# Kernel optimization log

Hardware: AMD Instinct MI355X
Metric: run time of the kernel (lower is better)

## Reference

```python
import jax, jax.numpy as jnp
import numpy as np

D_MODEL = 1024
NUM_HEADS = 16
HEAD_DIM = D_MODEL // NUM_HEADS
MASK_FUTURE = False
NEG_INF = -1.0e9


def setup_inputs() -> dict:
    key = jax.random.key(0)
    ks = jax.random.split(key, 8)
    B, L = 2, 2048
    q = jax.random.normal(ks[0], (B, L, D_MODEL), dtype=jnp.float32)
    k = jax.random.normal(ks[1], (B, L, D_MODEL), dtype=jnp.float32)
    v = jax.random.normal(ks[2], (B, L, D_MODEL), dtype=jnp.float32)
    attention_mask = jnp.ones((B, L), dtype=jnp.int32)
    s = 1.0 / np.sqrt(D_MODEL)
    Wq = jax.random.normal(ks[3], (D_MODEL, D_MODEL), dtype=jnp.float32) * s
    Wk = jax.random.normal(ks[4], (D_MODEL, D_MODEL), dtype=jnp.float32) * s
    Wv = jax.random.normal(ks[5], (D_MODEL, D_MODEL), dtype=jnp.float32) * s
    Wo = jax.random.normal(ks[6], (D_MODEL, D_MODEL), dtype=jnp.float32) * s
    return {"q": q, "k": k, "v": v, "attention_mask": attention_mask,
            "Wq": Wq, "Wk": Wk, "Wv": Wv, "Wo": Wo}


def _split_heads(x):
    B, L, _ = x.shape
    return x.reshape(B, L, NUM_HEADS, HEAD_DIM).transpose(0, 2, 1, 3)  # [B,H,L,Hd]


def reference(q, k, v, attention_mask, Wq, Wk, Wv, Wo):
    B, Lq, _ = q.shape
    Lk = k.shape[1]
    Q = _split_heads(q @ Wq.T)
    K = _split_heads(k @ Wk.T)
    V = _split_heads(v @ Wv.T)
    scale = HEAD_DIM ** 0.5  # per-head D in original Attention
    scores = jnp.einsum('bhqd,bhkd->bhqk', Q, K) / scale
    mask = (attention_mask == 0)[:, None, None, :]  # [B,1,1,Lk]
    scores = jnp.where(mask, NEG_INF, scores)
    if MASK_FUTURE:
        fut = jnp.triu(jnp.ones((Lq, Lk), dtype=bool), k=1)
        scores = jnp.where(fut[None, None], NEG_INF, scores)
    attn = jax.nn.softmax(scores, axis=-1)
    out = jnp.einsum('bhqk,bhkd->bhqd', attn, V)
    out = out.transpose(0, 2, 1, 3).reshape(B, Lq, D_MODEL)
    return out @ Wo.T
```

## Files before the change

### kernel.cpp

```cpp
#include <hip/hip_runtime.h>


#define D_MODEL 1024
#define NH 16
#define HD 64
#define BATCH 2
#define SEQ 2048
#define MROWS (BATCH*SEQ)

typedef unsigned short u16;
typedef __bf16 bf16x8 __attribute__((ext_vector_type(8)));
typedef float f32x4 __attribute__((ext_vector_type(4)));
typedef float f32x16 __attribute__((ext_vector_type(16)));

__device__ __forceinline__ u16 f2bf(float f){
    __bf16 h = (__bf16)f;
    return __builtin_bit_cast(u16, h);
}
__device__ __forceinline__ float fast_exp2(float x){ return __builtin_amdgcn_exp2f(x); }

__device__ __forceinline__ void stage16(const void* g, void* l){
#if __has_builtin(__builtin_amdgcn_global_load_lds)
    __builtin_amdgcn_global_load_lds(
        (__attribute__((address_space(1))) void*)(unsigned long long)(g),
        (__attribute__((address_space(3))) void*)(unsigned int)(unsigned long long)(l),
        16, 0, 0);
#else
    *(uint4*)l = *(const uint4*)g;
#endif
}

__device__ __forceinline__ int detect_f32_block(const u16* q, int tid){
    __shared__ int flag;
    if (tid < 64){
        unsigned e = (q[2*tid]>>7)&0xFFu;
        bool hit = (e>=115u)&&(e<=132u);
        unsigned long long m = __ballot(hit);
        if (tid==0) flag = (__popcll(m) < 32) ? 1 : 0;
    }
    __syncthreads();
    return flag;
}

__global__ __launch_bounds__(256)
void convert_all(const u16* __restrict__ q, const u16* __restrict__ k,
                 const u16* __restrict__ v, const u16* __restrict__ Wq,
                 const u16* __restrict__ Wk, const u16* __restrict__ Wv,
                 const u16* __restrict__ Wo, u16* __restrict__ dst)
{
    int isf32 = detect_f32_block(q, threadIdx.x);
    int bid = blockIdx.x;
    const u16* src; int lb;
    if      (bid < 4096)  { src=q;  lb=bid; }
    else if (bid < 8192)  { src=k;  lb=bid-4096; }
    else if (bid < 12288) { src=v;  lb=bid-8192; }
    else if (bid < 13312) { src=Wq; lb=bid-12288; }
    else if (bid < 14336) { src=Wk; lb=bid-13312; }
    else if (bid < 15360) { src=Wv; lb=bid-14336; }
    else                  { src=Wo; lb=bid-15360; }
    size_t so = (size_t)lb*1024 + threadIdx.x*4;
    size_t dofs = (size_t)bid*1024 + threadIdx.x*4;
    if (isf32){
        float4 x = *(const float4*)((const float*)src + so);
        ushort4 o; o.x=f2bf(x.x); o.y=f2bf(x.y); o.z=f2bf(x.z); o.w=f2bf(x.w);
        *(ushort4*)(dst+dofs) = o;
    } else {
        *(ushort4*)(dst+dofs) = *(const ushort4*)(src+so);
    }
}

__global__ __launch_bounds__(512)
void gemm_qkv(const u16* __restrict__ qb, const u16* __restrict__ kb,
              const u16* __restrict__ vb, const u16* __restrict__ Wqb,
              const u16* __restrict__ Wkb, const u16* __restrict__ Wvb,
              u16* __restrict__ Qh, u16* __restrict__ Kh, u16* __restrict__ Vt)
{
    const int K = 1024;
    __shared__ __align__(16) u16 lA[2][128*64];
    __shared__ __align__(16) u16 lB[2][128*64];

    const int lid = blockIdx.x + 8*(blockIdx.y + 32*blockIdx.z);
    const int xcd = lid & 7, loc = lid >> 3;
    const int xb = loc & 7, p = loc >> 3;
    const int yz = xcd*12 + p;
    const int z = yz >> 5, yb = yz & 31;

    const u16* A  = (z==0)? qb  : (z==1)? kb  : vb;
    const u16* Bt = (z==0)? Wqb : (z==1)? Wkb : Wvb;

    const int tid  = threadIdx.x;
    const int wid  = tid>>6, lane = tid&63;
    const int quad = lane>>4, l16 = lane&15;
    const int wm = (wid&3)*32, wn = (wid>>2)*64;
    const int row0 = yb*128, col0 = xb*128;

    f32x4 acc[2][4];
    #pragma unroll
    for (int i=0;i<2;i++)
        #pragma unroll
        for (int j=0;j<4;j++) acc[i][j] = (f32x4){0.f,0.f,0.f,0.f};

    #define QKV_STAGE(buf, k0)                                                 \
        _Pragma("unroll")                                                      \
        for (int s=0;s<2;s++){                                                 \
            int c = tid + s*512;                                               \
            int row = c>>3, cr = c&7;                                          \
            int gc = cr ^ (row&7);                                             \
            stage16(&A [(size_t)(row0+row)*K + (k0) + gc*8], &lA[buf][c*8]);   \
            stage16(&Bt[(size_t)(col0+row)*K + (k0) + gc*8], &lB[buf][c*8]);   \
        }

    QKV_STAGE(0, 0)
    __syncthreads();

    int cur = 0;
    for (int t=0; t<16; ++t){
        if (t < 15) QKV_STAGE(cur^1, (t+1)*64)
        #pragma unroll
        for (int kk=0;kk<2;kk++){
            bf16x8 af[2], bfr[4];
            #pragma unroll
            for (int mi=0;mi<2;mi++){
                int r = wm + mi*16 + l16;
                af[mi] = *(const bf16x8*)&lA[cur][r*64 + ((kk*4+quad) ^ (r&7))*8];
            }
            #pragma unroll
            for (int ni=0;ni<4;ni++){
                int r = wn + ni*16 + l16;
                bfr[ni] = *(const bf16x8*)&lB[cur][r*64 + ((kk*4+quad) ^ (r&7))*8];
            }
            #pragma unroll
            for (int mi=0;mi<2;mi++)
                #pragma unroll
                for (int ni=0;ni<4;ni++)
                    acc[mi][ni] = __builtin_amdgcn_mfma_f32_16x16x32_bf16(af[mi], bfr[ni], acc[mi][ni], 0,0,0);
        }
        __syncthreads();
        cur ^= 1;
    }
    #undef QKV_STAGE

    const float qsc = (z==0) ? 0.18033688011112042f : 1.0f;
    u16* Csh = (z==0)? Qh : Kh;
    #pragma unroll
    for (int mi=0;mi<2;mi++){
        #pragma unroll
        for (int ni=0;ni<4;ni++){
            int col = col0 + wn + ni*16 + l16;
            #pragma unroll
            for (int r=0;r<4;r++){
                int row = row0 + wm + mi*16 + quad*4 + r;
                u16 o = f2bf(acc[mi][ni][r]*qsc);
                int b = row>>11, i = row&2047, h = col>>6, d = col&63;
                if (z<2) Csh[((((size_t)(b*NH+h))*SEQ + i)<<6) + d] = o;
                else     Vt[((size_t)((b*NH+h)*HD + d))*SEQ + i] = o;
            }
        }
    }
}

__global__ __launch_bounds__(512)
void gemm_out(const u16* __restrict__ A, const u16* __restrict__ Bt,
              void* __restrict__ Cv, const u16* __restrict__ qref)
{
    const int K = 1024, N = 1024;
    int outf32 = detect_f32_block(qref, threadIdx.x);
    __shared__ __align__(16) u16 lA[2][64*64];
    __shared__ __align__(16) u16 lB[2][128*64];
    const int tid  = threadIdx.x;
    const int wid  = tid>>6, lane = tid&63;
    const int quad = lane>>4, l16 = lane&15;
    const int wm = (wid&1)*32, wn = (wid>>1)*32;

    const int lid = blockIdx.x + 8*blockIdx.y;
    const int xcd = lid & 7, loc = lid >> 3;
    const int xb = loc & 7, yb = xcd*8 + (loc>>3);
    const int row0 = yb*64, col0 = xb*128;

    f32x4 acc[2][2];
    #pragma unroll
    for (int i=0;i<2;i++)
        #pragma unroll
        for (int j=0;j<2;j++) acc[i][j] = (f32x4){0.f,0.f,0.f,0.f};

    #define OUT_STAGE(buf, k0)                                                 \
        {                                                                      \
            int c2 = tid;                                                      \
            int row = c2>>3, cr = c2&7;                                        \
            int gc = cr ^ (row&7);                                             \
            stage16(&A[(size_t)(row0+row)*K + (k0) + gc*8], &lA[buf][c2*8]);   \
        }                                                                      \
        _Pragma("unroll")                                                      \
        for (int s=0;s<2;s++){                                                 \
            int c = tid + s*512;                                               \
            int row = c>>3, cr = c&7;                                          \
            int gc = cr ^ (row&7);                                             \
            stage16(&Bt[(size_t)(col0+row)*K + (k0) + gc*8], &lB[buf][c*8]);   \
        }

    OUT_STAGE(0, 0)
    __syncthreads();

    int cur = 0;
    for (int t=0; t<16; ++t){
        if (t < 15) OUT_STAGE(cur^1, (t+1)*64)
        #pragma unroll
        for (int kk=0;kk<2;kk++){
            bf16x8 af[2], bfr[2];
            #pragma unroll
            for (int mi=0;mi<2;mi++){
                int r = wm + mi*16 + l16;
                af[mi] = *(const bf16x8*)&lA[cur][r*64 + ((kk*4+quad) ^ (r&7))*8];
            }
            #pragma unroll
            for (int ni=0;ni<2;ni++){
                int r = wn + ni*16 + l16;
                bfr[ni] = *(const bf16x8*)&lB[cur][r*64 + ((kk*4+quad) ^ (r&7))*8];
            }
            #pragma unroll
            for (int mi=0;mi<2;mi++)
                #pragma unroll
                for (int ni=0;ni<2;ni++)
                    acc[mi][ni] = __builtin_amdgcn_mfma_f32_16x16x32_bf16(af[mi], bfr[ni], acc[mi][ni], 0,0,0);
        }
        __syncthreads();
        cur ^= 1;
    }
    #undef OUT_STAGE

    #pragma unroll
    for (int mi=0;mi<2;mi++){
        #pragma unroll
        for (int ni=0;ni<2;ni++){
            int col = col0 + wn + ni*16 + l16;
            #pragma unroll
            for (int r=0;r<4;r++){
                int row = row0 + wm + mi*16 + quad*4 + r;
                float f = acc[mi][ni][r];
                if (outf32) ((float*)Cv)[(size_t)row*N + col] = f;
                else        ((u16*)Cv)[(size_t)row*N + col] = f2bf(f);
            }
        }
    }
}

#define KVT 4096
#define VROW 68
#define VVT (64*VROW)
#define SW(row, c8) ((row)*64 + ((((c8) ^ ((row)&7)))*8))

__global__ __launch_bounds__(512, 4)
void attn3(const u16* __restrict__ Qh, const u16* __restrict__ Kh,
           const u16* __restrict__ Vt, const int* __restrict__ mask,
           u16* __restrict__ ctx)
{
    __shared__ __align__(16) u16 smem[4*KVT + 4*VVT];
    __shared__ unsigned mb[64];

    const int id = blockIdx.x;
    const int bh = (id&7)*4 + (id>>7);
    const int qb = (id>>3)&15;
    const int b = bh>>4, h = bh&15;
    const int i0 = qb*128;
    const int tid = threadIdx.x;
    const int wv = tid>>6, lane = tid&63;
    const int l31 = lane&31, hi = lane>>5;
    const int hf = tid>>8;
    const int lt = tid&255;
    const int wq = wv&3;

    u16* lkh = smem + (hf*2)*KVT;
    u16* lvh = smem + 4*KVT + (hf*2)*VVT;

    const u16* Kp  = Kh + (size_t)bh*SEQ*HD + (size_t)hf*1024*HD;
    const u16* Vtp = Vt + (size_t)bh*HD*SEQ + hf*1024;
    const int* mp  = mask + b*SEQ;

    if (tid < 64){
        unsigned w = 0;
        #pragma unroll 8
        for (int i=0;i<32;i++) w |= (mp[tid*32+i] ? 1u:0u) << i;
        mb[tid] = w;
    }
    #pragma unroll
    for (int s=0;s<2;s++){
        int c = lt + s*256;
        int r = c>>3, c8 = c&7;
        *(uint4*)&lkh[SW(r,c8)] = *(const uint4*)&Kp[(size_t)r*HD + c8*8];
        uint4 x = *(const uint4*)&Vtp[(size_t)r*SEQ + c8*8];
        uint2 xl; xl.x = x.x; xl.y = x.y;
        uint2 xh; xh.x = x.z; xh.y = x.w;
        *(uint2*)&lvh[r*VROW + c8*8]     = xl;
        *(uint2*)&lvh[r*VROW + c8*8 + 4] = xh;
    }

    const u16* Qrow = Qh + ((size_t)bh*SEQ + i0 + wq*32 + l31)*HD;
    bf16x8 aq[4];
    #pragma unroll
    for (int kk=0;kk<4;kk++) aq[kk] = *(const bf16x8*)&Qrow[kk*16 + hi*8];

    bf16x8 bones;
    #pragma unroll
    for (int j=0;j<8;j++) ((u16*)&bones)[j] = 0x3F80;

    f32x16 Oacc[2], Lacc;
    #pragma unroll
    for (int r=0;r<16;r++){ Oacc[0][r]=0.f; Oacc[1][r]=0.f; Lacc[r]=0.f; }

    for (int t=0; t<16; t++){
        u16* lkc = lkh + (t&1)*KVT;
        u16* lvc = lvh + (t&1)*VVT;
        u16* lkn = lkh + ((t&1)^1)*KVT;
        u16* lvn = lvh + ((t&1)^1)*VVT;

        __syncthreads();

        uint4 gk[2], gv[2];
        if (t < 15){
            #pragma unroll
            for (int s=0;s<2;s++){
                int c = lt + s*256;
                int r = c>>3, c8 = c&7;
                gk[s] = *(const uint4*)&Kp[(size_t)(t*64+64+r)*HD + c8*8];
                gv[s] = *(const uint4*)&Vtp[(size_t)r*SEQ + t*64+64 + c8*8];
            }
        }

        __builtin_amdgcn_s_setprio(1);
        #pragma unroll
        for (int jt=0; jt<2; ++jt){
            f32x16 sfr;
            #pragma unroll
            for (int r=0;r<16;r++) sfr[r]=0.f;
            #pragma unroll
            for (int kk=0;kk<4;kk++){
                bf16x8 ak = *(const bf16x8*)&lkc[SW(jt*32+l31, 2*kk+hi)];
                sfr = __builtin_amdgcn_mfma_f32_32x32x16_bf16(ak, aq[kk], sfr, 0,0,0);
            }

            unsigned mw = mb[(hf*16+t)*2 + jt];
            if ((unsigned)__builtin_amdgcn_readfirstlane((int)mw) != 0xFFFFFFFFu){
                unsigned ms = mw >> (hi*4);
                #pragma unroll
                for (int r=0;r<16;r++){
                    int kb = (r&3)+8*(r>>2);
                    if (!((ms>>kb)&1u)) sfr[r] = -1.0e9f;
                }
            }

            unsigned cc[8];
            #pragma unroll
            for (int d=0; d<8; ++d){
                float p0 = fast_exp2(sfr[2*d]);
                float p1 = fast_exp2(sfr[2*d+1]);
                cc[d] = (unsigned)f2bf(p0) | ((unsigned)f2bf(p1)<<16);
            }
            bf16x8 pa0, pa1;
            ((unsigned*)&pa0)[0]=cc[0]; ((unsigned*)&pa0)[1]=cc[1];
            ((unsigned*)&pa0)[2]=cc[2]; ((unsigned*)&pa0)[3]=cc[3];
            ((unsigned*)&pa1)[0]=cc[4]; ((unsigned*)&pa1)[1]=cc[5];
            ((unsigned*)&pa1)[2]=cc[6]; ((unsigned*)&pa1)[3]=cc[7];

            Lacc = __builtin_amdgcn_mfma_f32_32x32x16_bf16(pa0, bones, Lacc, 0,0,0);
            Lacc = __builtin_amdgcn_mfma_f32_32x32x16_bf16(pa1, bones, Lacc, 0,0,0);

            #pragma unroll
            for (int dn=0; dn<2; ++dn){
                int vrb = (dn*32 + l31)*VROW + jt*32 + 4*hi;
                uint2 a0 = *(const uint2*)&lvc[vrb];
                uint2 a1 = *(const uint2*)&lvc[vrb + 8];
                uint2 b0 = *(const uint2*)&lvc[vrb + 16];
                uint2 b1 = *(const uint2*)&lvc[vrb + 24];
                union { uint4 u; bf16x8 v; } bv0, bv1;
                bv0.u.x=a0.x; bv0.u.y=a0.y; bv0.u.z=a1.x; bv0.u.w=a1.y;
                bv1.u.x=b0.x; bv1.u.y=b0.y; bv1.u.z=b1.x; bv1.u.w=b1.y;
                Oacc[dn] = __builtin_amdgcn_mfma_f32_32x32x16_bf16(pa0, bv0.v, Oacc[dn], 0,0,0);
                Oacc[dn] = __builtin_amdgcn_mfma_f32_32x32x16_bf16(pa1, bv1.v, Oacc[dn], 0,0,0);
            }
        }
        __builtin_amdgcn_s_setprio(0);

        if (t < 15){
            #pragma unroll
            for (int s=0;s<2;s++){
                int c = lt + s*256;
                int r = c>>3, c8 = c&7;
                *(uint4*)&lkn[SW(r,c8)] = gk[s];
                uint2 xl; xl.x = gv[s].x; xl.y = gv[s].y;
                uint2 xh; xh.x = gv[s].z; xh.y = gv[s].w;
                *(uint2*)&lvn[r*VROW + c8*8]     = xl;
                *(uint2*)&lvn[r*VROW + c8*8 + 4] = xh;
            }
        }
    }

    __syncthreads();
    float* mrg = (float*)smem;
    if (hf == 1){
        float* p = mrg + (size_t)(wq*64 + lane)*49;
        #pragma unroll
        for (int dn=0; dn<2; ++dn)
            #pragma unroll
            for (int r=0;r<16;r++) p[dn*16+r] = Oacc[dn][r];
        #pragma unroll
        for (int r=0;r<16;r++) p[32+r] = Lacc[r];
    }
    __syncthreads();
    if (hf == 0){
        const float* p = mrg + (size_t)(wq*64 + lane)*49;
        #pragma unroll
        for (int dn=0; dn<2; ++dn)
            #pragma unroll
            for (int r=0;r<16;r++) Oacc[dn][r] += p[dn*16+r];
        float rc[16];
        #pragma unroll
        for (int r=0;r<16;r++) rc[r] = 1.0f / (Lacc[r] + p[32+r]);
        #pragma unroll
        for (int dn=0; dn<2; ++dn){
            int col = h*HD + dn*32 + l31;
            #pragma unroll
            for (int r=0;r<16;r++){
                int row = i0 + wq*32 + (r&3) + 8*(r>>2) + 4*hi;
                ctx[((size_t)(b*SEQ+row))*D_MODEL + col] = f2bf(Oacc[dn][r] * rc[r]);
            }
        }
    }
}

extern "C" void kernel_launch(void* const* d_in, const int* in_sizes, int n_in,
                              void* d_out, int out_size, void* d_ws, size_t ws_size,
                              hipStream_t stream)
{
    (void)in_sizes; (void)n_in; (void)out_size; (void)ws_size;
    const u16* q    = (const u16*)d_in[0];
    const u16* k    = (const u16*)d_in[1];
    const u16* v    = (const u16*)d_in[2];
    const int* mask = (const int*)d_in[3];
    const u16* Wq   = (const u16*)d_in[4];
    const u16* Wk   = (const u16*)d_in[5];
    const u16* Wv   = (const u16*)d_in[6];
    const u16* Wo   = (const u16*)d_in[7];

    const size_t TEN = (size_t)MROWS * D_MODEL;
    const size_t WEL = (size_t)D_MODEL * D_MODEL;
    u16* qb  = (u16*)d_ws;
    u16* kb  = qb + TEN;
    u16* vb  = kb + TEN;
    u16* Wqb = vb + TEN;
    u16* Wkb = Wqb + WEL;
    u16* Wvb = Wkb + WEL;
    u16* Wob = Wvb + WEL;
    u16* Qh  = Wob + WEL;
    u16* Kh  = Qh + TEN;
    u16* Vtr = Kh + TEN;
    u16* ctx = Vtr + TEN;

    dim3 bb(256);
    convert_all<<<dim3(16384), bb, 0, stream>>>(q,k,v,Wq,Wk,Wv,Wo, qb);
    gemm_qkv<<<dim3(8,32,3), dim3(512), 0, stream>>>(qb,kb,vb, Wqb,Wkb,Wvb, Qh,Kh,Vtr);
    attn3<<<dim3(512), dim3(512), 0, stream>>>(Qh, Kh, Vtr, mask, ctx);
    gemm_out<<<dim3(8,64), dim3(512), 0, stream>>>(ctx, Wob, d_out, q);
}
```

Measured before the change: 215.6 us.

## Single-buffer K/V tiles in LDS to halve shared memory and raise occupancy

Replaces the double-buffered K/V LDS tiles with single buffers, adding barriers around the refill so the next tile is written only after all waves finish reading the current one. The final cross-half merge is split into two smaller phases so it fits in the reduced shared-memory footprint. The launch-bounds occupancy hint is raised so more blocks can be resident per CU. In exchange, each iteration gains extra block-wide syncs, and LDS writes of the next tile no longer overlap with compute on the current tile.

```diff
diff --git a/kernel.cpp b/kernel.cpp
--- a/kernel.cpp
+++ b/kernel.cpp
@@ -249,12 +249,12 @@
 #define VVT (64*VROW)
 #define SW(row, c8) ((row)*64 + ((((c8) ^ ((row)&7)))*8))
 
-__global__ __launch_bounds__(512, 4)
+__global__ __launch_bounds__(512, 8)
 void attn3(const u16* __restrict__ Qh, const u16* __restrict__ Kh,
            const u16* __restrict__ Vt, const int* __restrict__ mask,
            u16* __restrict__ ctx)
 {
-    __shared__ __align__(16) u16 smem[4*KVT + 4*VVT];
+    __shared__ __align__(16) u16 smem[2*KVT + 2*VVT];
     __shared__ unsigned mb[64];
 
     const int id = blockIdx.x;
@@ -269,8 +269,8 @@
     const int lt = tid&255;
     const int wq = wv&3;
 
-    u16* lkh = smem + (hf*2)*KVT;
-    u16* lvh = smem + 4*KVT + (hf*2)*VVT;
+    u16* lk = smem + hf*KVT;
+    u16* lv = smem + 2*KVT + hf*VVT;
 
     const u16* Kp  = Kh + (size_t)bh*SEQ*HD + (size_t)hf*1024*HD;
     const u16* Vtp = Vt + (size_t)bh*HD*SEQ + hf*1024;
@@ -286,12 +286,12 @@
     for (int s=0;s<2;s++){
         int c = lt + s*256;
         int r = c>>3, c8 = c&7;
-        *(uint4*)&lkh[SW(r,c8)] = *(const uint4*)&Kp[(size_t)r*HD + c8*8];
+        *(uint4*)&lk[SW(r,c8)] = *(const uint4*)&Kp[(size_t)r*HD + c8*8];
         uint4 x = *(const uint4*)&Vtp[(size_t)r*SEQ + c8*8];
         uint2 xl; xl.x = x.x; xl.y = x.y;
         uint2 xh; xh.x = x.z; xh.y = x.w;
-        *(uint2*)&lvh[r*VROW + c8*8]     = xl;
-        *(uint2*)&lvh[r*VROW + c8*8 + 4] = xh;
+        *(uint2*)&lv[r*VROW + c8*8]     = xl;
+        *(uint2*)&lv[r*VROW + c8*8 + 4] = xh;
     }
 
     const u16* Qrow = Qh + ((size_t)bh*SEQ + i0 + wq*32 + l31)*HD;
@@ -307,14 +307,9 @@
     #pragma unroll
     for (int r=0;r<16;r++){ Oacc[0][r]=0.f; Oacc[1][r]=0.f; Lacc[r]=0.f; }
 
+    __syncthreads();
+
     for (int t=0; t<16; t++){
-        u16* lkc = lkh + (t&1)*KVT;
-        u16* lvc = lvh + (t&1)*VVT;
-        u16* lkn = lkh + ((t&1)^1)*KVT;
-        u16* lvn = lvh + ((t&1)^1)*VVT;
-
-        __syncthreads();
-
         uint4 gk[2], gv[2];
         if (t < 15){
             #pragma unroll
@@ -334,7 +329,7 @@
             for (int r=0;r<16;r++) sfr[r]=0.f;
             #pragma unroll
             for (int kk=0;kk<4;kk++){
-                bf16x8 ak = *(const bf16x8*)&lkc[SW(jt*32+l31, 2*kk+hi)];
+                bf16x8 ak = *(const bf16x8*)&lk[SW(jt*32+l31, 2*kk+hi)];
                 sfr = __builtin_amdgcn_mfma_f32_32x32x16_bf16(ak, aq[kk], sfr, 0,0,0);
             }
 
@@ -367,10 +362,10 @@
             #pragma unroll
             for (int dn=0; dn<2; ++dn){
                 int vrb = (dn*32 + l31)*VROW + jt*32 + 4*hi;
-                uint2 a0 = *(const uint2*)&lvc[vrb];
-                uint2 a1 = *(const uint2*)&lvc[vrb + 8];
-                uint2 b0 = *(const uint2*)&lvc[vrb + 16];
-                uint2 b1 = *(const uint2*)&lvc[vrb + 24];
+                uint2 a0 = *(const uint2*)&lv[vrb];
+                uint2 a1 = *(const uint2*)&lv[vrb + 8];
+                uint2 b0 = *(const uint2*)&lv[vrb + 16];
+                uint2 b1 = *(const uint2*)&lv[vrb + 24];
                 union { uint4 u; bf16x8 v; } bv0, bv1;
                 bv0.u.x=a0.x; bv0.u.y=a0.y; bv0.u.z=a1.x; bv0.u.w=a1.y;
                 bv1.u.x=b0.x; bv1.u.y=b0.y; bv1.u.z=b1.x; bv1.u.w=b1.y;
@@ -381,40 +376,54 @@
         __builtin_amdgcn_s_setprio(0);
 
         if (t < 15){
+            __syncthreads();
             #pragma unroll
             for (int s=0;s<2;s++){
                 int c = lt + s*256;
                 int r = c>>3, c8 = c&7;
-                *(uint4*)&lkn[SW(r,c8)] = gk[s];
+                *(uint4*)&lk[SW(r,c8)] = gk[s];
                 uint2 xl; xl.x = gv[s].x; xl.y = gv[s].y;
                 uint2 xh; xh.x = gv[s].z; xh.y = gv[s].w;
-                *(uint2*)&lvn[r*VROW + c8*8]     = xl;
-                *(uint2*)&lvn[r*VROW + c8*8 + 4] = xh;
-            }
+                *(uint2*)&lv[r*VROW + c8*8]     = xl;
+                *(uint2*)&lv[r*VROW + c8*8 + 4] = xh;
+            }
+            __syncthreads();
         }
     }
 
     __syncthreads();
     float* mrg = (float*)smem;
+    const int slot = wq*64 + lane;
+    float lm[16];
     if (hf == 1){
-        float* p = mrg + (size_t)(wq*64 + lane)*49;
-        #pragma unroll
-        for (int dn=0; dn<2; ++dn)
-            #pragma unroll
-            for (int r=0;r<16;r++) p[dn*16+r] = Oacc[dn][r];
-        #pragma unroll
-        for (int r=0;r<16;r++) p[32+r] = Lacc[r];
+        float* p = mrg + (size_t)slot*33;
+        #pragma unroll
+        for (int r=0;r<16;r++) p[r]    = Oacc[0][r];
+        #pragma unroll
+        for (int r=0;r<16;r++) p[16+r] = Lacc[r];
     }
     __syncthreads();
     if (hf == 0){
-        const float* p = mrg + (size_t)(wq*64 + lane)*49;
-        #pragma unroll
-        for (int dn=0; dn<2; ++dn)
-            #pragma unroll
-            for (int r=0;r<16;r++) Oacc[dn][r] += p[dn*16+r];
+        const float* p = mrg + (size_t)slot*33;
+        #pragma unroll
+        for (int r=0;r<16;r++) Oacc[0][r] += p[r];
+        #pragma unroll
+        for (int r=0;r<16;r++) lm[r] = Lacc[r] + p[16+r];
+    }
+    __syncthreads();
+    if (hf == 1){
+        float* p = mrg + (size_t)slot*17;
+        #pragma unroll
+        for (int r=0;r<16;r++) p[r] = Oacc[1][r];
+    }
+    __syncthreads();
+    if (hf == 0){
+        const float* p = mrg + (size_t)slot*17;
+        #pragma unroll
+        for (int r=0;r<16;r++) Oacc[1][r] += p[r];
         float rc[16];
         #pragma unroll
-        for (int r=0;r<16;r++) rc[r] = 1.0f / (Lacc[r] + p[32+r]);
+        for (int r=0;r<16;r++) rc[r] = 1.0f / lm[r];
         #pragma unroll
         for (int dn=0; dn<2; ++dn){
             int col = h*HD + dn*32 + l31;
```

Measured after the change: 525.6 us. 2.44x slower.
